# Kernel tuning notes

Hardware: AMD Instinct MI355X
Metric: run time of the kernel (lower is better)

Reference implementation:

```python
import jax, jax.numpy as jnp
import numpy as np

N = 384
NEG = jnp.float32(-1e30)


def setup_inputs() -> dict:
    key = jax.random.key(0)
    k1, k2, k3 = jax.random.split(key, 3)
    od = jax.random.uniform(k1, (N, N), dtype=jnp.float32) * 100.0  # OD demand (nn.Parameter in torch)
    adj = jax.random.randint(k2, (N, N), 0, 2, dtype=jnp.int32)     # binary adjacency
    dist = jax.random.uniform(k3, (N, N), dtype=jnp.float32) * 10.0 + 1.0  # free-flow times t0
    return {"od": od, "adj": adj, "dist": dist, "lambda_param": 1, "capacity": 500}


def _logit_assignment(od, adj, dist, lam):
    # Vectorized equivalent of the torch nested-loop logit assignment.
    # Paths have cutoff=2 edges: direct (o->d) and two-hop (o->k->d, k!=o, k!=d).
    n = od.shape[0]
    eye = jnp.eye(n, dtype=bool)
    # demand gated by od>0; diagonal OD pairs contribute no edge flow
    demand = jnp.where((od > 0) & ~eye, od, 0.0)
    A = (adj > 0) & ~eye  # usable directed edges (self-loops never on a simple path)
    # direct-path logits [o,d]
    l1 = jnp.where(A, -lam * dist, NEG)
    # two-hop path mask/times [o,k,d]; simple path => k!=o (in A), k!=d (in A), o!=d
    hop = A[:, :, None] & A[None, :, :] & (~eye)[:, None, :]
    t2 = dist[:, :, None] + dist[None, :, :]
    l2 = jnp.where(hop, -lam * t2, NEG)
    # stable softmax over {direct} u {all k} per OD pair
    m = jnp.maximum(l1, l2.max(axis=1))  # [o,d]
    e1 = jnp.where(A, jnp.exp(l1 - m), 0.0)
    e2 = jnp.where(hop, jnp.exp(l2 - m[:, None, :]), 0.0)
    Z = e1 + e2.sum(axis=1)  # [o,d]
    safe = Z > 0
    w = jnp.where(safe, demand / jnp.where(safe, Z, 1.0), 0.0)  # demand * (1/Z)
    # scatter assigned flow onto edges
    flows = w * e1                                       # direct edge (o,d)
    flows = flows + jnp.einsum('od,okd->ok', w, e2)      # first hop edge (o,k)
    flows = flows + jnp.einsum('od,okd->kd', w, e2)      # second hop edge (k,d)
    return flows


def reference(od, adj, dist, lambda_param, capacity):
    # max_iter=1 in the source, and the post-assignment BPR travel-time update is
    # under no_grad and only mutates G after the single assignment, so the returned
    # flow_results equals one logit assignment on the free-flow distances.
    lam = jnp.float32(lambda_param)
    return _logit_assignment(od, adj, dist, lam)
```

## Files before the change

kernel.cpp:

```cpp
#include <hip/hip_runtime.h>
#include <math.h>

#define NN 384
#define NT 24
#define NTILES (NT * NT)

typedef __attribute__((ext_vector_type(8))) short short8;
typedef __attribute__((ext_vector_type(4))) float v4f;

__device__ __forceinline__ unsigned short f2bf(float f) {
    union { float f; unsigned u; } v; v.f = f;
    unsigned r = (v.u + 0x7FFFu + ((v.u >> 16) & 1u)) >> 16;
    return (unsigned short)r;
}
__device__ __forceinline__ float bf2f(unsigned short h) {
    union { unsigned u; float f; } v; v.u = ((unsigned)h) << 16;
    return v.f;
}

__global__ void build_p_kernel(const int* __restrict__ adj,
                               const float* __restrict__ dist,
                               const int* __restrict__ lam_ptr,
                               unsigned short* __restrict__ P16,
                               unsigned short* __restrict__ PT16) {
    int idx = blockIdx.x * 256 + threadIdx.x;
    int i = idx / NN;
    int j = idx - i * NN;
    float lam = (float)(*lam_ptr);
    float p = (adj[idx] > 0 && i != j) ? expf(-lam * dist[idx]) : 0.0f;
    unsigned short h = f2bf(p);
    P16[idx] = h;
    PT16[j * NN + i] = h;
}

__global__ __launch_bounds__(64) void v_kernel(const unsigned short* __restrict__ P16,
                                               const unsigned short* __restrict__ PT16,
                                               const float* __restrict__ od,
                                               float* __restrict__ V32,
                                               unsigned short* __restrict__ V16,
                                               unsigned short* __restrict__ VT16) {
    int t = blockIdx.x;
    int i0 = (t / NT) * 16, j0 = (t % NT) * 16;
    int lane = threadIdx.x;
    int col = lane & 15, quad = lane >> 4;
    v4f acc = {0.f, 0.f, 0.f, 0.f};
    const short8* arow = (const short8*)(P16 + (i0 + col) * NN + quad * 8);
    const short8* brow = (const short8*)(PT16 + (j0 + col) * NN + quad * 8);
#pragma unroll
    for (int k0 = 0; k0 < NN / 32; ++k0) {
        short8 a = arow[k0 * 4];
        short8 b = brow[k0 * 4];
        acc = __builtin_amdgcn_mfma_f32_16x16x32_bf16(a, b, acc, 0, 0, 0);
    }
#pragma unroll
    for (int r = 0; r < 4; ++r) {
        int i = i0 + quad * 4 + r, j = j0 + col;
        int idx = i * NN + j;
        float denom = bf2f(P16[idx]) + acc[r];
        float o = od[idx];
        float v = (i != j && o > 0.0f && denom > 0.0f) ? o / denom : 0.0f;
        V32[idx] = v;
        unsigned short h = f2bf(v);
        V16[idx] = h;
        VT16[j * NN + i] = h;
    }
}

__global__ __launch_bounds__(64) void flows_kernel(const unsigned short* __restrict__ P16,
                                                   const unsigned short* __restrict__ PT16,
                                                   const unsigned short* __restrict__ V16,
                                                   const unsigned short* __restrict__ VT16,
                                                   const float* __restrict__ V32,
                                                   const int* __restrict__ adj,
                                                   const float* __restrict__ dist,
                                                   const int* __restrict__ lam_ptr,
                                                   float* __restrict__ out) {
    int t = blockIdx.x;
    int i0 = (t / NT) * 16, j0 = (t % NT) * 16;
    int lane = threadIdx.x;
    int col = lane & 15, quad = lane >> 4;
    v4f accW = {0.f, 0.f, 0.f, 0.f};
    v4f accU = {0.f, 0.f, 0.f, 0.f};
    const short8* aW = (const short8*)(V16 + (i0 + col) * NN + quad * 8);
    const short8* bW = (const short8*)(P16 + (j0 + col) * NN + quad * 8);
    const short8* aU = (const short8*)(PT16 + (i0 + col) * NN + quad * 8);
    const short8* bU = (const short8*)(VT16 + (j0 + col) * NN + quad * 8);
#pragma unroll
    for (int k0 = 0; k0 < NN / 32; ++k0) {
        short8 a0 = aW[k0 * 4];
        short8 b0 = bW[k0 * 4];
        short8 a1 = aU[k0 * 4];
        short8 b1 = bU[k0 * 4];
        accW = __builtin_amdgcn_mfma_f32_16x16x32_bf16(a0, b0, accW, 0, 0, 0);
        accU = __builtin_amdgcn_mfma_f32_16x16x32_bf16(a1, b1, accU, 0, 0, 0);
    }
    float lam = (float)(*lam_ptr);
#pragma unroll
    for (int r = 0; r < 4; ++r) {
        int i = i0 + quad * 4 + r, j = j0 + col;
        int idx = i * NN + j;
        float p = (adj[idx] > 0 && i != j) ? expf(-lam * dist[idx]) : 0.0f;
        out[idx] = p * (V32[idx] + accW[r] + accU[r]);
    }
}

extern "C" void kernel_launch(void* const* d_in, const int* in_sizes, int n_in,
                              void* d_out, int out_size, void* d_ws, size_t ws_size,
                              hipStream_t stream) {
    const float* od   = (const float*)d_in[0];
    const int*   adj  = (const int*)d_in[1];
    const float* dist = (const float*)d_in[2];
    const int*   lam  = (const int*)d_in[3];
    float* out = (float*)d_out;

    unsigned short* P16  = (unsigned short*)d_ws;
    unsigned short* PT16 = P16 + NN * NN;
    unsigned short* V16  = PT16 + NN * NN;
    unsigned short* VT16 = V16 + NN * NN;
    float*          V32  = (float*)(VT16 + NN * NN);

    build_p_kernel<<<NTILES, 256, 0, stream>>>(adj, dist, lam, P16, PT16);
    v_kernel<<<NTILES, 64, 0, stream>>>(P16, PT16, od, V32, V16, VT16);
    flows_kernel<<<NTILES, 64, 0, stream>>>(P16, PT16, V16, VT16, V32, adj, dist, lam, out);
}
```

Before: 75.57 us.

## Fuse three kernels into one cooperative kernel with grid syncs

Replaces the three separate launches with one cooperative kernel of 144 blocks of 256 threads, using grid.sync between the P-build, V-compute and flows phases. The P-build phase is vectorised, uses __expf, and stores fp32 P so later phases no longer recompute exp or reread adj/dist. V and P stay in registers across phases, which drops the V32 buffer. The aim is to remove launch overhead and redundant work, at the cost of grid-wide barrier latency and lower parallelism per phase.

New measurement: 126.0 us. +66.7%, slower.

```diff
diff --git a/kernel.cpp b/kernel.cpp
--- a/kernel.cpp
+++ b/kernel.cpp
@@ -1,106 +1,113 @@
 #include <hip/hip_runtime.h>
+#include <hip/hip_cooperative_groups.h>
 #include <math.h>
+
+namespace cg = cooperative_groups;
 
 #define NN 384
 #define NT 24
 #define NTILES (NT * NT)
+#define NBLK 144
+#define TPB 256
 
 typedef __attribute__((ext_vector_type(8))) short short8;
 typedef __attribute__((ext_vector_type(4))) float v4f;
+typedef __attribute__((ext_vector_type(4))) int int4v;
+typedef __attribute__((ext_vector_type(4))) float float4v;
+typedef __attribute__((ext_vector_type(4))) short short4v;
 
 __device__ __forceinline__ unsigned short f2bf(float f) {
     union { float f; unsigned u; } v; v.f = f;
-    unsigned r = (v.u + 0x7FFFu + ((v.u >> 16) & 1u)) >> 16;
-    return (unsigned short)r;
-}
-__device__ __forceinline__ float bf2f(unsigned short h) {
-    union { unsigned u; float f; } v; v.u = ((unsigned)h) << 16;
-    return v.f;
+    return (unsigned short)((v.u + 0x7FFFu + ((v.u >> 16) & 1u)) >> 16);
 }
 
-__global__ void build_p_kernel(const int* __restrict__ adj,
-                               const float* __restrict__ dist,
-                               const int* __restrict__ lam_ptr,
-                               unsigned short* __restrict__ P16,
-                               unsigned short* __restrict__ PT16) {
-    int idx = blockIdx.x * 256 + threadIdx.x;
-    int i = idx / NN;
-    int j = idx - i * NN;
-    float lam = (float)(*lam_ptr);
-    float p = (adj[idx] > 0 && i != j) ? expf(-lam * dist[idx]) : 0.0f;
-    unsigned short h = f2bf(p);
-    P16[idx] = h;
-    PT16[j * NN + i] = h;
-}
+__global__ __launch_bounds__(TPB) void fused(
+    const float* __restrict__ od, const int* __restrict__ adj,
+    const float* __restrict__ dist, const int* __restrict__ lam_ptr,
+    float* __restrict__ out,
+    unsigned short* __restrict__ P16, unsigned short* __restrict__ PT16,
+    unsigned short* __restrict__ V16, unsigned short* __restrict__ VT16,
+    float* __restrict__ P32)
+{
+    cg::grid_group grid = cg::this_grid();
+    const float lam = (float)(*lam_ptr);
 
-__global__ __launch_bounds__(64) void v_kernel(const unsigned short* __restrict__ P16,
-                                               const unsigned short* __restrict__ PT16,
-                                               const float* __restrict__ od,
-                                               float* __restrict__ V32,
-                                               unsigned short* __restrict__ V16,
-                                               unsigned short* __restrict__ VT16) {
-    int t = blockIdx.x;
-    int i0 = (t / NT) * 16, j0 = (t % NT) * 16;
-    int lane = threadIdx.x;
-    int col = lane & 15, quad = lane >> 4;
-    v4f acc = {0.f, 0.f, 0.f, 0.f};
-    const short8* arow = (const short8*)(P16 + (i0 + col) * NN + quad * 8);
-    const short8* brow = (const short8*)(PT16 + (j0 + col) * NN + quad * 8);
+    {
+        int tid = blockIdx.x * TPB + threadIdx.x;
+        int idx0 = tid * 4;
+        int i = idx0 / NN;
+        int jb = idx0 - i * NN;
+        int4v   a4 = *(const int4v*)(adj + idx0);
+        float4v d4 = *(const float4v*)(dist + idx0);
+        float4v p4;
+        short4v h4;
 #pragma unroll
-    for (int k0 = 0; k0 < NN / 32; ++k0) {
-        short8 a = arow[k0 * 4];
-        short8 b = brow[k0 * 4];
-        acc = __builtin_amdgcn_mfma_f32_16x16x32_bf16(a, b, acc, 0, 0, 0);
+        for (int u = 0; u < 4; ++u) {
+            int j = jb + u;
+            float p = (a4[u] > 0 && i != j) ? __expf(-lam * d4[u]) : 0.0f;
+            p4[u] = p;
+            unsigned short h = f2bf(p);
+            h4[u] = (short)h;
+            PT16[j * NN + i] = h;
+        }
+        *(float4v*)(P32 + idx0) = p4;
+        *(short4v*)((short*)P16 + idx0) = h4;
     }
+
+    grid.sync();
+
+    const int t = blockIdx.x * 4 + (threadIdx.x >> 6);
+    const int lane = threadIdx.x & 63;
+    const int i0 = (t / NT) * 16, j0 = (t % NT) * 16;
+    const int col = lane & 15, quad = lane >> 4;
+
+    float pv[4], vv[4];
+
+    {
+        v4f acc0 = {0.f, 0.f, 0.f, 0.f};
+        v4f acc1 = {0.f, 0.f, 0.f, 0.f};
+        const short8* arow = (const short8*)(P16 + (i0 + col) * NN + quad * 8);
+        const short8* brow = (const short8*)(PT16 + (j0 + col) * NN + quad * 8);
 #pragma unroll
-    for (int r = 0; r < 4; ++r) {
-        int i = i0 + quad * 4 + r, j = j0 + col;
-        int idx = i * NN + j;
-        float denom = bf2f(P16[idx]) + acc[r];
-        float o = od[idx];
-        float v = (i != j && o > 0.0f && denom > 0.0f) ? o / denom : 0.0f;
-        V32[idx] = v;
-        unsigned short h = f2bf(v);
-        V16[idx] = h;
-        VT16[j * NN + i] = h;
+        for (int k0 = 0; k0 < NN / 64; ++k0) {
+            acc0 = __builtin_amdgcn_mfma_f32_16x16x32_bf16(arow[k0 * 8],     brow[k0 * 8],     acc0, 0, 0, 0);
+            acc1 = __builtin_amdgcn_mfma_f32_16x16x32_bf16(arow[k0 * 8 + 4], brow[k0 * 8 + 4], acc1, 0, 0, 0);
+        }
+#pragma unroll
+        for (int r = 0; r < 4; ++r) {
+            int i = i0 + quad * 4 + r, j = j0 + col;
+            int idx = i * NN + j;
+            float p = P32[idx];
+            float denom = p + acc0[r] + acc1[r];
+            float o = od[idx];
+            float v = (i != j && o > 0.0f && denom > 0.0f) ? o / denom : 0.0f;
+            pv[r] = p;
+            vv[r] = v;
+            unsigned short h = f2bf(v);
+            V16[idx] = h;
+            VT16[j * NN + i] = h;
+        }
     }
-}
 
-__global__ __launch_bounds__(64) void flows_kernel(const unsigned short* __restrict__ P16,
-                                                   const unsigned short* __restrict__ PT16,
-                                                   const unsigned short* __restrict__ V16,
-                                                   const unsigned short* __restrict__ VT16,
-                                                   const float* __restrict__ V32,
-                                                   const int* __restrict__ adj,
-                                                   const float* __restrict__ dist,
-                                                   const int* __restrict__ lam_ptr,
-                                                   float* __restrict__ out) {
-    int t = blockIdx.x;
-    int i0 = (t / NT) * 16, j0 = (t % NT) * 16;
-    int lane = threadIdx.x;
-    int col = lane & 15, quad = lane >> 4;
-    v4f accW = {0.f, 0.f, 0.f, 0.f};
-    v4f accU = {0.f, 0.f, 0.f, 0.f};
-    const short8* aW = (const short8*)(V16 + (i0 + col) * NN + quad * 8);
-    const short8* bW = (const short8*)(P16 + (j0 + col) * NN + quad * 8);
-    const short8* aU = (const short8*)(PT16 + (i0 + col) * NN + quad * 8);
-    const short8* bU = (const short8*)(VT16 + (j0 + col) * NN + quad * 8);
+    grid.sync();
+
+    {
+        v4f accW = {0.f, 0.f, 0.f, 0.f};
+        v4f accU = {0.f, 0.f, 0.f, 0.f};
+        const short8* aW = (const short8*)(V16  + (i0 + col) * NN + quad * 8);
+        const short8* bW = (const short8*)(P16  + (j0 + col) * NN + quad * 8);
+        const short8* aU = (const short8*)(PT16 + (i0 + col) * NN + quad * 8);
+        const short8* bU = (const short8*)(VT16 + (j0 + col) * NN + quad * 8);
 #pragma unroll
-    for (int k0 = 0; k0 < NN / 32; ++k0) {
-        short8 a0 = aW[k0 * 4];
-        short8 b0 = bW[k0 * 4];
-        short8 a1 = aU[k0 * 4];
-        short8 b1 = bU[k0 * 4];
-        accW = __builtin_amdgcn_mfma_f32_16x16x32_bf16(a0, b0, accW, 0, 0, 0);
-        accU = __builtin_amdgcn_mfma_f32_16x16x32_bf16(a1, b1, accU, 0, 0, 0);
-    }
-    float lam = (float)(*lam_ptr);
+        for (int k0 = 0; k0 < NN / 32; ++k0) {
+            accW = __builtin_amdgcn_mfma_f32_16x16x32_bf16(aW[k0 * 4], bW[k0 * 4], accW, 0, 0, 0);
+            accU = __builtin_amdgcn_mfma_f32_16x16x32_bf16(aU[k0 * 4], bU[k0 * 4], accU, 0, 0, 0);
+        }
 #pragma unroll
-    for (int r = 0; r < 4; ++r) {
-        int i = i0 + quad * 4 + r, j = j0 + col;
-        int idx = i * NN + j;
-        float p = (adj[idx] > 0 && i != j) ? expf(-lam * dist[idx]) : 0.0f;
-        out[idx] = p * (V32[idx] + accW[r] + accU[r]);
+        for (int r = 0; r < 4; ++r) {
+            int i = i0 + quad * 4 + r, j = j0 + col;
+            out[i * NN + j] = pv[r] * (vv[r] + accW[r] + accU[r]);
+        }
     }
 }
 
@@ -117,9 +124,9 @@
     unsigned short* PT16 = P16 + NN * NN;
     unsigned short* V16  = PT16 + NN * NN;
     unsigned short* VT16 = V16 + NN * NN;
-    float*          V32  = (float*)(VT16 + NN * NN);
+    float*          P32  = (float*)(VT16 + NN * NN);
 
-    build_p_kernel<<<NTILES, 256, 0, stream>>>(adj, dist, lam, P16, PT16);
-    v_kernel<<<NTILES, 64, 0, stream>>>(P16, PT16, od, V32, V16, VT16);
-    flows_kernel<<<NTILES, 64, 0, stream>>>(P16, PT16, V16, VT16, V32, adj, dist, lam, out);
+    void* args[] = {(void*)&od, (void*)&adj, (void*)&dist, (void*)&lam, (void*)&out,
+                    (void*)&P16, (void*)&PT16, (void*)&V16, (void*)&VT16, (void*)&P32};
+    hipLaunchCooperativeKernel((void*)fused, dim3(NBLK), dim3(TPB), args, 0, stream);
 }
```

## Fuse P construction into V GEMM with LDS-staged 32x32 tiles

Applied to the files above, without the earlier changes.

Merges the P-building kernel and the V GEMM kernel into one kernel. Each 256-thread block recomputes the P rows and columns it needs directly into padded shared memory, then runs MFMA from LDS on a 32x32 output tile split across four waves. Blocks on the first tile row and column also write P and PT to global memory for the flows kernel. This removes one launch and the global round trip for P, at the cost of redundant exp work across blocks, fewer blocks (144), and a switch to the fast __expf.

Result: slower. 81.32 us (+7.6%).

```diff
diff --git a/kernel.cpp b/kernel.cpp
--- a/kernel.cpp
+++ b/kernel.cpp
@@ -4,59 +4,114 @@
 #define NN 384
 #define NT 24
 #define NTILES (NT * NT)
+#define PAD 392
 
 typedef __attribute__((ext_vector_type(8))) short short8;
 typedef __attribute__((ext_vector_type(4))) float v4f;
+typedef __attribute__((ext_vector_type(4))) int int4v;
+typedef __attribute__((ext_vector_type(4))) float float4v;
+typedef __attribute__((ext_vector_type(4))) short short4v;
 
 __device__ __forceinline__ unsigned short f2bf(float f) {
     union { float f; unsigned u; } v; v.f = f;
-    unsigned r = (v.u + 0x7FFFu + ((v.u >> 16) & 1u)) >> 16;
-    return (unsigned short)r;
-}
-__device__ __forceinline__ float bf2f(unsigned short h) {
-    union { unsigned u; float f; } v; v.u = ((unsigned)h) << 16;
-    return v.f;
+    return (unsigned short)((v.u + 0x7FFFu + ((v.u >> 16) & 1u)) >> 16);
 }
 
-__global__ void build_p_kernel(const int* __restrict__ adj,
-                               const float* __restrict__ dist,
-                               const int* __restrict__ lam_ptr,
-                               unsigned short* __restrict__ P16,
-                               unsigned short* __restrict__ PT16) {
-    int idx = blockIdx.x * 256 + threadIdx.x;
-    int i = idx / NN;
-    int j = idx - i * NN;
-    float lam = (float)(*lam_ptr);
-    float p = (adj[idx] > 0 && i != j) ? expf(-lam * dist[idx]) : 0.0f;
-    unsigned short h = f2bf(p);
-    P16[idx] = h;
-    PT16[j * NN + i] = h;
-}
+__global__ __launch_bounds__(256) void pv_kernel(
+    const float* __restrict__ od, const int* __restrict__ adj,
+    const float* __restrict__ dist, const int* __restrict__ lam_ptr,
+    unsigned short* __restrict__ P16, unsigned short* __restrict__ PT16,
+    unsigned short* __restrict__ V16, unsigned short* __restrict__ VT16,
+    float* __restrict__ V32)
+{
+    __shared__ __align__(16) unsigned short As[32][PAD];
+    __shared__ __align__(16) unsigned short Bs[32][PAD];
 
-__global__ __launch_bounds__(64) void v_kernel(const unsigned short* __restrict__ P16,
-                                               const unsigned short* __restrict__ PT16,
-                                               const float* __restrict__ od,
-                                               float* __restrict__ V32,
-                                               unsigned short* __restrict__ V16,
-                                               unsigned short* __restrict__ VT16) {
-    int t = blockIdx.x;
-    int i0 = (t / NT) * 16, j0 = (t % NT) * 16;
-    int lane = threadIdx.x;
-    int col = lane & 15, quad = lane >> 4;
-    v4f acc = {0.f, 0.f, 0.f, 0.f};
-    const short8* arow = (const short8*)(P16 + (i0 + col) * NN + quad * 8);
-    const short8* brow = (const short8*)(PT16 + (j0 + col) * NN + quad * 8);
+    const int SI = blockIdx.x / 12, SJ = blockIdx.x % 12;
+    const int i0 = SI * 32, j0 = SJ * 32;
+    const float lam = (float)(*lam_ptr);
+    const int t = threadIdx.x;
+
+    {
+        const int m = t >> 3, ko = (t & 7) * 48;
+        const int gi = i0 + m;
+        const float4v* dp = (const float4v*)(dist + gi * NN + ko);
+        const int4v*   ap = (const int4v*)(adj + gi * NN + ko);
 #pragma unroll
-    for (int k0 = 0; k0 < NN / 32; ++k0) {
-        short8 a = arow[k0 * 4];
-        short8 b = brow[k0 * 4];
-        acc = __builtin_amdgcn_mfma_f32_16x16x32_bf16(a, b, acc, 0, 0, 0);
+        for (int u = 0; u < 12; ++u) {
+            float4v d4 = dp[u];
+            int4v   a4 = ap[u];
+            short4v h4;
+#pragma unroll
+            for (int v = 0; v < 4; ++v) {
+                int j = ko + u * 4 + v;
+                float p = (a4[v] > 0 && gi != j) ? __expf(-lam * d4[v]) : 0.0f;
+                h4[v] = (short)f2bf(p);
+            }
+            *(short4v*)&As[m][ko + u * 4] = h4;
+        }
+    }
+
+    {
+        const int half = t & 1;
+        const int kb = t >> 1;
+#pragma unroll
+        for (int pp = 0; pp < 3; ++pp) {
+            int k = pp * 128 + kb;
+            const float4v* dp = (const float4v*)(dist + k * NN + j0 + half * 16);
+            const int4v*   ap = (const int4v*)(adj + k * NN + j0 + half * 16);
+#pragma unroll
+            for (int q = 0; q < 4; ++q) {
+                float4v d4 = dp[q];
+                int4v   a4 = ap[q];
+#pragma unroll
+                for (int v = 0; v < 4; ++v) {
+                    int n = half * 16 + q * 4 + v;
+                    int j = j0 + n;
+                    float p = (a4[v] > 0 && k != j) ? __expf(-lam * d4[v]) : 0.0f;
+                    Bs[n][k] = f2bf(p);
+                }
+            }
+        }
+    }
+
+    __syncthreads();
+
+    if (SJ == 0) {
+        const int m = t >> 3, ko = (t & 7) * 48;
+#pragma unroll
+        for (int u = 0; u < 12; ++u)
+            *(short4v*)(P16 + (i0 + m) * NN + ko + u * 4) = *(short4v*)&As[m][ko + u * 4];
+    }
+    if (SI == 0) {
+        const int n = t >> 3, ko = (t & 7) * 48;
+#pragma unroll
+        for (int u = 0; u < 12; ++u)
+            *(short4v*)(PT16 + (j0 + n) * NN + ko + u * 4) = *(short4v*)&Bs[n][ko + u * 4];
+    }
+
+    const int w = t >> 6, lane = t & 63;
+    const int wi = w >> 1, wj = w & 1;
+    const int col = lane & 15, quad = lane >> 4;
+    const unsigned short* arow = &As[wi * 16 + col][0];
+    const unsigned short* brow = &Bs[wj * 16 + col][0];
+    v4f acc0 = {0.f, 0.f, 0.f, 0.f};
+    v4f acc1 = {0.f, 0.f, 0.f, 0.f};
+#pragma unroll
+    for (int k0 = 0; k0 < NN / 64; ++k0) {
+        short8 a0 = *(const short8*)(arow + k0 * 64 + quad * 8);
+        short8 b0 = *(const short8*)(brow + k0 * 64 + quad * 8);
+        short8 a1 = *(const short8*)(arow + k0 * 64 + 32 + quad * 8);
+        short8 b1 = *(const short8*)(brow + k0 * 64 + 32 + quad * 8);
+        acc0 = __builtin_amdgcn_mfma_f32_16x16x32_bf16(a0, b0, acc0, 0, 0, 0);
+        acc1 = __builtin_amdgcn_mfma_f32_16x16x32_bf16(a1, b1, acc1, 0, 0, 0);
     }
 #pragma unroll
     for (int r = 0; r < 4; ++r) {
-        int i = i0 + quad * 4 + r, j = j0 + col;
+        int i = i0 + wi * 16 + quad * 4 + r, j = j0 + wj * 16 + col;
         int idx = i * NN + j;
-        float denom = bf2f(P16[idx]) + acc[r];
+        float p = (adj[idx] > 0 && i != j) ? __expf(-lam * dist[idx]) : 0.0f;
+        float denom = p + acc0[r] + acc1[r];
         float o = od[idx];
         float v = (i != j && o > 0.0f && denom > 0.0f) ? o / denom : 0.0f;
         V32[idx] = v;
@@ -99,7 +154,7 @@
     for (int r = 0; r < 4; ++r) {
         int i = i0 + quad * 4 + r, j = j0 + col;
         int idx = i * NN + j;
-        float p = (adj[idx] > 0 && i != j) ? expf(-lam * dist[idx]) : 0.0f;
+        float p = (adj[idx] > 0 && i != j) ? __expf(-lam * dist[idx]) : 0.0f;
         out[idx] = p * (V32[idx] + accW[r] + accU[r]);
     }
 }
@@ -119,7 +174,6 @@
     unsigned short* VT16 = V16 + NN * NN;
     float*          V32  = (float*)(VT16 + NN * NN);
 
-    build_p_kernel<<<NTILES, 256, 0, stream>>>(adj, dist, lam, P16, PT16);
-    v_kernel<<<NTILES, 64, 0, stream>>>(P16, PT16, od, V32, V16, VT16);
+    pv_kernel<<<144, 256, 0, stream>>>(od, adj, dist, lam, P16, PT16, V16, VT16, V32);
     flows_kernel<<<NTILES, 64, 0, stream>>>(P16, PT16, V16, VT16, V32, adj, dist, lam, out);
 }
```
